# Kernel optimization log

Hardware: AMD Instinct MI355X
Metric: run time of the kernel (lower is better)

Reference implementation:

```python
import jax, jax.numpy as jnp
import numpy as np

B, N, D, H, L = 512, 50000, 64, 600, 200
ALPHA = 1.0
EPS_NORM = 1e-12


def _l2n(x):
    # matches tf.linalg.l2_normalize / keras.backend.l2_normalize (axis=-1)
    return x * jax.lax.rsqrt(jnp.maximum(jnp.sum(x * x, axis=-1, keepdims=True), EPS_NORM))


def setup_inputs() -> dict:
    key = jax.random.key(0)
    ks = jax.random.split(key, 8)
    inputs = jax.random.randint(ks[0], (B, N), 0, 2).astype(jnp.float32)
    item_emb = jax.random.normal(ks[1], (N, D), jnp.float32) * 0.1
    W1 = jax.random.normal(ks[2], (N + D, H), jnp.float32) * 0.01
    Wm = jax.random.normal(ks[3], (H, L), jnp.float32) * 0.05
    Wv = jax.random.normal(ks[4], (H, L), jnp.float32) * 0.05
    Wd1 = jax.random.normal(ks[5], (L, H), jnp.float32) * 0.05
    Wd2 = jax.random.normal(ks[6], (H, N), jnp.float32) * 0.01
    eps = jax.random.normal(ks[7], (B, L), jnp.float32)
    return {
        "inputs": inputs, "item_emb": item_emb,
        "W1": W1, "b1": jnp.zeros((H,), jnp.float32),
        "Wm": Wm, "bm": jnp.zeros((L,), jnp.float32),
        "Wv": Wv, "bv": jnp.zeros((L,), jnp.float32),
        "Wd1": Wd1, "bd1": jnp.zeros((H,), jnp.float32),
        "Wd2": Wd2, "bd2": jnp.zeros((N,), jnp.float32),
        "eps": eps,
    }


def reference(inputs, item_emb, W1, b1, Wm, bm, Wv, bv, Wd1, bd1, Wd2, bd2, eps):
    # --- vectorized replacement of tf.map_fn row-wise masked gather + mean pool ---
    mask = (inputs > 0).astype(inputs.dtype)            # [B, N]
    cnt = jnp.maximum(jnp.sum(mask, axis=-1, keepdims=True), 1.0)
    pooled = (mask @ item_emb) / cnt                    # [B, D] mean of selected item embeddings
    x = jnp.concatenate([inputs, ALPHA * _l2n(pooled)], axis=-1)  # [B, N+D]
    # --- encoder ---
    xn = _l2n(x)                                        # l2 normalize over axis=1
    h = jnp.tanh(xn @ W1 + b1)                          # [B, H]
    z_mean = h @ Wm + bm                                # [B, L]
    z_log_var = h @ Wv + bv                             # [B, L]
    z = z_mean + jnp.exp(0.5 * z_log_var) * eps         # reparameterization
    # --- decoder ---
    reconstructed = jnp.tanh(z @ Wd1 + bd1) @ Wd2 + bd2  # [B, N]
    kl_loss = -0.5 * jnp.mean(z_log_var - jnp.square(z_mean) - jnp.exp(z_log_var) + 1.0)
    return reconstructed, kl_loss
```

## Files before the change

### kernel.cpp

```cpp
#include <hip/hip_runtime.h>

#define BB 512
#define NN 50000
#define DD 64
#define HH 600
#define LL 200

#define K1 50176
#define S1 1568
#define N1P 704
#define NCH 28
#define CKE 1792
#define CW 56
#define NST 14

#define K2P 640
#define N2P 50048

typedef __attribute__((ext_vector_type(8))) short bf16x8;
typedef __attribute__((ext_vector_type(4))) float f32x4;

__device__ __forceinline__ unsigned short f2bf(float f) {
  union { float f; unsigned u; } v; v.f = f;
  unsigned r = v.u + 0x7fffu + ((v.u >> 16) & 1u);
  return (unsigned short)(r >> 16);
}

__device__ __forceinline__ void g2l16(const void* g, void* l) {
  __builtin_amdgcn_global_load_lds((const __attribute__((address_space(1))) unsigned int*)g,
                                   (__attribute__((address_space(3))) unsigned int*)l, 16, 0, 0);
}

__global__ __launch_bounds__(256) void k_prep(const float* __restrict__ inp,
                                              unsigned* __restrict__ maskT,
                                              float* __restrict__ cnt,
                                              float* __restrict__ P,
                                              float* __restrict__ outkl) {
  int b = blockIdx.x, tid = threadIdx.x;
  const float4* row4 = (const float4*)(inp + (size_t)b * NN);
  int c = 0;
  for (int w = tid; w < S1; w += 256) {
    unsigned m = 0;
    int kb = w * 32;
    if (kb + 32 <= NN) {
#pragma unroll
      for (int q = 0; q < 8; ++q) {
        float4 f = row4[w * 8 + q];
        m |= (f.x > 0.5f ? 1u : 0u) << (4 * q);
        m |= (f.y > 0.5f ? 1u : 0u) << (4 * q + 1);
        m |= (f.z > 0.5f ? 1u : 0u) << (4 * q + 2);
        m |= (f.w > 0.5f ? 1u : 0u) << (4 * q + 3);
      }
    } else {
      for (int k = kb; k < NN && k < kb + 32; ++k)
        m |= (inp[(size_t)b * NN + k] > 0.5f ? 1u : 0u) << (k - kb);
    }
    maskT[(size_t)w * BB + b] = m;
    c += __popc(m);
  }
  __shared__ int sred[256];
  sred[tid] = c; __syncthreads();
  for (int s = 128; s > 0; s >>= 1) { if (tid < s) sred[tid] += sred[tid + s]; __syncthreads(); }
  if (tid == 0) cnt[b] = (float)sred[0];
  for (int j = tid; j < N1P; j += 256) P[(size_t)b * N1P + j] = 0.f;
  if (b == 0 && tid == 0) *outkl = 0.f;
}

__global__ __launch_bounds__(256) void k_convB1(const float* __restrict__ W1,
                                                const float* __restrict__ item_emb,
                                                unsigned short* __restrict__ BT) {
  __shared__ unsigned short lds[64][65];
  int k0 = blockIdx.x * 64, j0 = blockIdx.y * 64;
  int tx = threadIdx.x & 63, ty = threadIdx.x >> 6;
  int j = j0 + tx;
#pragma unroll
  for (int r = 0; r < 16; ++r) {
    int k = k0 + ty + 4 * r;
    float v = 0.f;
    if (k < NN) {
      if (j < HH) v = W1[(size_t)k * HH + j];
      else if (j < HH + DD) v = item_emb[(size_t)k * DD + (j - HH)];
    }
    lds[tx][ty + 4 * r] = f2bf(v);
  }
  __syncthreads();
#pragma unroll
  for (int r = 0; r < 16; ++r) {
    int jj = j0 + ty + 4 * r;
    int kk = k0 + tx;
    BT[(size_t)jj * K1 + kk] = lds[ty + 4 * r][tx];
  }
}

__global__ __launch_bounds__(256) void k_convB2(const float* __restrict__ Wd2,
                                                unsigned short* __restrict__ WT) {
  __shared__ unsigned short lds[64][65];
  int n0 = blockIdx.x * 64, k0 = blockIdx.y * 64;
  int tx = threadIdx.x & 63, ty = threadIdx.x >> 6;
  int n = n0 + tx;
#pragma unroll
  for (int r = 0; r < 16; ++r) {
    int k = k0 + ty + 4 * r;
    float v = 0.f;
    if (k < HH && n < NN) v = Wd2[(size_t)k * NN + n];
    lds[tx][ty + 4 * r] = f2bf(v);
  }
  __syncthreads();
#pragma unroll
  for (int r = 0; r < 16; ++r) {
    int nn = n0 + ty + 4 * r;
    int kk = k0 + tx;
    WT[(size_t)nn * K2P + kk] = lds[ty + 4 * r][tx];
  }
}

__global__ __launch_bounds__(512) void k_gemm1(const unsigned* __restrict__ maskT,
                                               const unsigned short* __restrict__ BT,
                                               float* __restrict__ P) {
  __shared__ unsigned short sB[2 * 8192];
  __shared__ unsigned sM[2 * 2048];
  int tid = threadIdx.x;
  int wave = tid >> 6, lane = tid & 63;
  int lr = lane & 15, kg = lane >> 4;
  int n0 = blockIdx.x * 64;
  int m0 = wave * 64;
  int cK = blockIdx.y * CKE;
  int cWo = blockIdx.y * CW;

  auto stage = [&](int p, int st) {
    int kb = cK + st * 128;
#pragma unroll
    for (int i = 0; i < 2; ++i) {
      int row = wave * 8 + i * 4 + kg;
      int cbs = (lr * 16) ^ ((row & 7) << 4);
      const unsigned short* src = BT + (size_t)(n0 + row) * K1 + kb + (cbs >> 1);
      unsigned short* dst = sB + p * 8192 + wave * 1024 + i * 512;
      g2l16(src, dst);
    }
    int w0 = cWo + st * 4;
    const unsigned* msrc = maskT + (size_t)w0 * BB + wave * 256 + lane * 4;
    unsigned* mdst = sM + p * 2048 + wave * 256;
    g2l16(msrc, mdst);
  };

  stage(0, 0);
  f32x4 acc[4][4] = {};

  for (int st = 0; st < NST; ++st) {
    int cur = st & 1;
    if (st + 1 < NST) {
      stage(cur ^ 1, st + 1);
      asm volatile("s_waitcnt vmcnt(3)" ::: "memory");
    } else {
      asm volatile("s_waitcnt vmcnt(0)" ::: "memory");
    }
    __builtin_amdgcn_s_barrier();

    const unsigned short* Bb = sB + cur * 8192;
    const unsigned* Mb = sM + cur * 2048;
#pragma unroll
    for (int ks = 0; ks < 4; ++ks) {
      bf16x8 b[4];
#pragma unroll
      for (int j = 0; j < 4; ++j) {
        int row = j * 16 + lr;
        int cb = (ks * 64 + kg * 16) ^ ((row & 7) << 4);
        b[j] = *(const bf16x8*)(Bb + row * 128 + (cb >> 1));
      }
#pragma unroll
      for (int i = 0; i < 4; ++i) {
        unsigned mw = Mb[ks * 512 + m0 + i * 16 + lr];
        unsigned byt = (mw >> (kg * 8)) & 0xFFu;
        union { unsigned u[4]; bf16x8 v; } au;
#pragma unroll
        for (int p2 = 0; p2 < 4; ++p2) {
          unsigned t = (byt >> (2 * p2)) & 3u;
          t = (t | (t << 15)) & 0x10001u;
          au.u[p2] = t * 0x3F80u;
        }
#pragma unroll
        for (int j = 0; j < 4; ++j)
          acc[i][j] = __builtin_amdgcn_mfma_f32_16x16x32_bf16(au.v, b[j], acc[i][j], 0, 0, 0);
      }
    }
    __builtin_amdgcn_s_barrier();
  }

  int row0 = (lane >> 4) * 4, col = lane & 15;
#pragma unroll
  for (int i = 0; i < 4; ++i)
#pragma unroll
    for (int j = 0; j < 4; ++j)
#pragma unroll
      for (int r = 0; r < 4; ++r)
        atomicAdd(&P[(size_t)(m0 + i * 16 + row0 + r) * N1P + (n0 + j * 16 + col)], acc[i][j][r]);
}

__global__ __launch_bounds__(256) void k_mid(const float* __restrict__ P,
                                             const float* __restrict__ cntb,
                                             const float* __restrict__ W1,
                                             const float* __restrict__ b1,
                                             const float* __restrict__ Wm,
                                             const float* __restrict__ bm,
                                             const float* __restrict__ Wv,
                                             const float* __restrict__ bv,
                                             const float* __restrict__ Wd1,
                                             const float* __restrict__ bd1,
                                             const float* __restrict__ eps,
                                             unsigned short* __restrict__ TB,
                                             float* __restrict__ outkl) {
  int b = blockIdx.x, tid = threadIdx.x;
  __shared__ float pn[DD];
  __shared__ float h[HH];
  __shared__ float z[LL];
  __shared__ float red[1];
  __shared__ float sred[256];

  float cnt = cntb[b];
  if (tid < 64) {
    float pooled = P[(size_t)b * N1P + HH + tid] / fmaxf(cnt, 1.f);
    float s2 = pooled * pooled;
    for (int o = 32; o > 0; o >>= 1) s2 += __shfl_xor(s2, o);
    float pnv = pooled * rsqrtf(fmaxf(s2, 1e-12f));
    pn[tid] = pnv;
    float p2 = pnv * pnv;
    for (int o = 32; o > 0; o >>= 1) p2 += __shfl_xor(p2, o);
    if (tid == 0) red[0] = rsqrtf(fmaxf(cnt + p2, 1e-12f));
  }
  __syncthreads();
  float inv = red[0];

  for (int j = tid; j < HH; j += 256) {
    float corr = 0.f;
#pragma unroll 8
    for (int d = 0; d < DD; ++d) corr += pn[d] * W1[(size_t)(NN + d) * HH + j];
    h[j] = tanhf((P[(size_t)b * N1P + j] + corr) * inv + b1[j]);
  }
  __syncthreads();

  float klp = 0.f;
  for (int l = tid; l < LL; l += 256) {
    float zm = bm[l], zv = bv[l];
    for (int j = 0; j < HH; ++j) {
      float hv = h[j];
      zm += hv * Wm[(size_t)j * LL + l];
      zv += hv * Wv[(size_t)j * LL + l];
    }
    z[l] = zm + expf(0.5f * zv) * eps[(size_t)b * LL + l];
    klp += zv - zm * zm - expf(zv) + 1.f;
  }
  sred[tid] = klp; __syncthreads();
  for (int s = 128; s > 0; s >>= 1) { if (tid < s) sred[tid] += sred[tid + s]; __syncthreads(); }
  if (tid == 0) atomicAdd(outkl, sred[0] * (-0.5f / (float)(BB * LL)));

  for (int j = tid; j < K2P; j += 256) {
    unsigned short o = 0;
    if (j < HH) {
      float acc = bd1[j];
      for (int l = 0; l < LL; ++l) acc += z[l] * Wd1[(size_t)l * HH + j];
      o = f2bf(tanhf(acc));
    }
    TB[(size_t)b * K2P + j] = o;
  }
}

__global__ __launch_bounds__(512) void k_gemm2(const unsigned short* __restrict__ T,
                                               const unsigned short* __restrict__ WT,
                                               const float* __restrict__ bd2,
                                               float* __restrict__ out) {
  __shared__ unsigned short sB[2 * 8192];
  int tid = threadIdx.x;
  int wave = tid >> 6, lane = tid & 63;
  int lr = lane & 15, kg = lane >> 4;
  int n0 = blockIdx.x * 64;
  int m0 = wave * 64;

  auto stage = [&](int p, int st) {
    int kb = st * 128;
#pragma unroll
    for (int i = 0; i < 2; ++i) {
      int row = wave * 8 + i * 4 + kg;
      int cbs = (lr * 16) ^ ((row & 7) << 4);
      const unsigned short* src = WT + (size_t)(n0 + row) * K2P + kb + (cbs >> 1);
      unsigned short* dst = sB + p * 8192 + wave * 1024 + i * 512;
      g2l16(src, dst);
    }
  };

  stage(0, 0);
  f32x4 acc[4][4] = {};

  for (int st = 0; st < 5; ++st) {
    int cur = st & 1;
    if (st + 1 < 5) {
      stage(cur ^ 1, st + 1);
      asm volatile("s_waitcnt vmcnt(2)" ::: "memory");
    } else {
      asm volatile("s_waitcnt vmcnt(0)" ::: "memory");
    }
    __builtin_amdgcn_s_barrier();

    const unsigned short* Bb = sB + cur * 8192;
#pragma unroll
    for (int ks = 0; ks < 4; ++ks) {
      bf16x8 a[4], b[4];
#pragma unroll
      for (int i = 0; i < 4; ++i)
        a[i] = *(const bf16x8*)(T + (size_t)(m0 + i * 16 + lr) * K2P + st * 128 + ks * 32 + kg * 8);
#pragma unroll
      for (int j = 0; j < 4; ++j) {
        int row = j * 16 + lr;
        int cb = (ks * 64 + kg * 16) ^ ((row & 7) << 4);
        b[j] = *(const bf16x8*)(Bb + row * 128 + (cb >> 1));
      }
#pragma unroll
      for (int i = 0; i < 4; ++i)
#pragma unroll
        for (int j = 0; j < 4; ++j)
          acc[i][j] = __builtin_amdgcn_mfma_f32_16x16x32_bf16(a[i], b[j], acc[i][j], 0, 0, 0);
    }
    __builtin_amdgcn_s_barrier();
  }

  int row0 = (lane >> 4) * 4, col = lane & 15;
#pragma unroll
  for (int i = 0; i < 4; ++i)
#pragma unroll
    for (int j = 0; j < 4; ++j) {
      int n = n0 + j * 16 + col;
      if (n < NN) {
        float bias = bd2[n];
#pragma unroll
        for (int r = 0; r < 4; ++r) {
          int m = m0 + i * 16 + row0 + r;
          out[(size_t)m * NN + n] = acc[i][j][r] + bias;
        }
      }
    }
}

extern "C" void kernel_launch(void* const* d_in, const int* in_sizes, int n_in,
                              void* d_out, int out_size, void* d_ws, size_t ws_size,
                              hipStream_t stream) {
  (void)in_sizes; (void)n_in; (void)out_size; (void)ws_size;
  const float* inputs   = (const float*)d_in[0];
  const float* item_emb = (const float*)d_in[1];
  const float* W1  = (const float*)d_in[2];
  const float* b1  = (const float*)d_in[3];
  const float* Wm  = (const float*)d_in[4];
  const float* bm  = (const float*)d_in[5];
  const float* Wv  = (const float*)d_in[6];
  const float* bv  = (const float*)d_in[7];
  const float* Wd1 = (const float*)d_in[8];
  const float* bd1 = (const float*)d_in[9];
  const float* Wd2 = (const float*)d_in[10];
  const float* bd2 = (const float*)d_in[11];
  const float* eps = (const float*)d_in[12];
  float* out = (float*)d_out;

  char* ws = (char*)d_ws;
  unsigned* maskT     = (unsigned*)(ws + 0ull);
  unsigned short* BT1 = (unsigned short*)(ws + 3211264ull);
  unsigned short* W2T = (unsigned short*)(ws + 73859072ull);
  float* P            = (float*)(ws + 137920512ull);
  unsigned short* TB  = (unsigned short*)(ws + 139362304ull);
  float* cnt          = (float*)(ws + 140017664ull);

  float* outkl = out + (size_t)BB * NN;

  k_prep  <<<dim3(BB),       dim3(256), 0, stream>>>(inputs, maskT, cnt, P, outkl);
  k_convB1<<<dim3(784, 11),  dim3(256), 0, stream>>>(W1, item_emb, BT1);
  k_convB2<<<dim3(782, 10),  dim3(256), 0, stream>>>(Wd2, W2T);
  k_gemm1 <<<dim3(11, NCH),  dim3(512), 0, stream>>>(maskT, BT1, P);
  k_mid   <<<dim3(BB),       dim3(256), 0, stream>>>(P, cnt, W1, b1, Wm, bm, Wv, bv, Wd1, bd1, eps, TB, outkl);
  k_gemm2 <<<dim3(782),      dim3(512), 0, stream>>>(TB, W2T, bd2, out);
}
```

Measured before the change: 704.4 us.

## Prefetch mask and A operands into registers, double the K-split chunks

```diff
diff --git a/kernel.cpp b/kernel.cpp
--- a/kernel.cpp
+++ b/kernel.cpp
@@ -9,10 +9,10 @@
 #define K1 50176
 #define S1 1568
 #define N1P 704
-#define NCH 28
-#define CKE 1792
-#define CW 56
-#define NST 14
+#define NCH 56
+#define CKE 896
+#define CW 28
+#define NST 7
 
 #define K2P 640
 #define N2P 50048
@@ -118,7 +118,6 @@
                                                const unsigned short* __restrict__ BT,
                                                float* __restrict__ P) {
   __shared__ unsigned short sB[2 * 8192];
-  __shared__ unsigned sM[2 * 2048];
   int tid = threadIdx.x;
   int wave = tid >> 6, lane = tid & 63;
   int lr = lane & 15, kg = lane >> 4;
@@ -127,37 +126,43 @@
   int cK = blockIdx.y * CKE;
   int cWo = blockIdx.y * CW;
 
-  auto stage = [&](int p, int st) {
+  auto stageB = [&](int p, int st) {
     int kb = cK + st * 128;
 #pragma unroll
     for (int i = 0; i < 2; ++i) {
       int row = wave * 8 + i * 4 + kg;
       int cbs = (lr * 16) ^ ((row & 7) << 4);
-      const unsigned short* src = BT + (size_t)(n0 + row) * K1 + kb + (cbs >> 1);
-      unsigned short* dst = sB + p * 8192 + wave * 1024 + i * 512;
-      g2l16(src, dst);
-    }
+      g2l16(BT + (size_t)(n0 + row) * K1 + kb + (cbs >> 1),
+            sB + p * 8192 + wave * 1024 + i * 512);
+    }
+  };
+  auto loadM = [&](unsigned* mr, int st) {
     int w0 = cWo + st * 4;
-    const unsigned* msrc = maskT + (size_t)w0 * BB + wave * 256 + lane * 4;
-    unsigned* mdst = sM + p * 2048 + wave * 256;
-    g2l16(msrc, mdst);
+#pragma unroll
+    for (int ks = 0; ks < 4; ++ks)
+#pragma unroll
+      for (int i = 0; i < 4; ++i)
+        mr[ks * 4 + i] = maskT[(size_t)(w0 + ks) * BB + m0 + i * 16 + lr];
   };
 
-  stage(0, 0);
+  unsigned mC[16], mN[16];
+  stageB(0, 0);
+  loadM(mC, 0);
   f32x4 acc[4][4] = {};
 
+#pragma unroll
   for (int st = 0; st < NST; ++st) {
     int cur = st & 1;
     if (st + 1 < NST) {
-      stage(cur ^ 1, st + 1);
-      asm volatile("s_waitcnt vmcnt(3)" ::: "memory");
+      stageB(cur ^ 1, st + 1);
+      loadM(mN, st + 1);
+      asm volatile("s_waitcnt vmcnt(18)" ::: "memory");
     } else {
       asm volatile("s_waitcnt vmcnt(0)" ::: "memory");
     }
     __builtin_amdgcn_s_barrier();
 
     const unsigned short* Bb = sB + cur * 8192;
-    const unsigned* Mb = sM + cur * 2048;
 #pragma unroll
     for (int ks = 0; ks < 4; ++ks) {
       bf16x8 b[4];
@@ -169,8 +174,7 @@
       }
 #pragma unroll
       for (int i = 0; i < 4; ++i) {
-        unsigned mw = Mb[ks * 512 + m0 + i * 16 + lr];
-        unsigned byt = (mw >> (kg * 8)) & 0xFFu;
+        unsigned byt = (mC[ks * 4 + i] >> (kg * 8)) & 0xFFu;
         union { unsigned u[4]; bf16x8 v; } au;
 #pragma unroll
         for (int p2 = 0; p2 < 4; ++p2) {
@@ -184,6 +188,8 @@
       }
     }
     __builtin_amdgcn_s_barrier();
+#pragma unroll
+    for (int q = 0; q < 16; ++q) mC[q] = mN[q];
   }
 
   int row0 = (lane >> 4) * 4, col = lane & 15;
@@ -275,26 +281,36 @@
   int n0 = blockIdx.x * 64;
   int m0 = wave * 64;
 
-  auto stage = [&](int p, int st) {
+  auto stageB = [&](int p, int st) {
     int kb = st * 128;
 #pragma unroll
     for (int i = 0; i < 2; ++i) {
       int row = wave * 8 + i * 4 + kg;
       int cbs = (lr * 16) ^ ((row & 7) << 4);
-      const unsigned short* src = WT + (size_t)(n0 + row) * K2P + kb + (cbs >> 1);
-      unsigned short* dst = sB + p * 8192 + wave * 1024 + i * 512;
-      g2l16(src, dst);
+      g2l16(WT + (size_t)(n0 + row) * K2P + kb + (cbs >> 1),
+            sB + p * 8192 + wave * 1024 + i * 512);
     }
   };
-
-  stage(0, 0);
+  auto loadA = [&](bf16x8* a, int st) {
+#pragma unroll
+    for (int ks = 0; ks < 4; ++ks)
+#pragma unroll
+      for (int i = 0; i < 4; ++i)
+        a[ks * 4 + i] = *(const bf16x8*)(T + (size_t)(m0 + i * 16 + lr) * K2P + st * 128 + ks * 32 + kg * 8);
+  };
+
+  bf16x8 aC[16], aN[16];
+  stageB(0, 0);
+  loadA(aC, 0);
   f32x4 acc[4][4] = {};
 
+#pragma unroll
   for (int st = 0; st < 5; ++st) {
     int cur = st & 1;
     if (st + 1 < 5) {
-      stage(cur ^ 1, st + 1);
-      asm volatile("s_waitcnt vmcnt(2)" ::: "memory");
+      stageB(cur ^ 1, st + 1);
+      loadA(aN, st + 1);
+      asm volatile("s_waitcnt vmcnt(18)" ::: "memory");
     } else {
       asm volatile("s_waitcnt vmcnt(0)" ::: "memory");
     }
@@ -303,10 +319,7 @@
     const unsigned short* Bb = sB + cur * 8192;
 #pragma unroll
     for (int ks = 0; ks < 4; ++ks) {
-      bf16x8 a[4], b[4];
-#pragma unroll
-      for (int i = 0; i < 4; ++i)
-        a[i] = *(const bf16x8*)(T + (size_t)(m0 + i * 16 + lr) * K2P + st * 128 + ks * 32 + kg * 8);
+      bf16x8 b[4];
 #pragma unroll
       for (int j = 0; j < 4; ++j) {
         int row = j * 16 + lr;
@@ -317,9 +330,11 @@
       for (int i = 0; i < 4; ++i)
 #pragma unroll
         for (int j = 0; j < 4; ++j)
-          acc[i][j] = __builtin_amdgcn_mfma_f32_16x16x32_bf16(a[i], b[j], acc[i][j], 0, 0, 0);
+          acc[i][j] = __builtin_amdgcn_mfma_f32_16x16x32_bf16(aC[ks * 4 + i], b[j], acc[i][j], 0, 0, 0);
     }
     __builtin_amdgcn_s_barrier();
+#pragma unroll
+    for (int q = 0; q < 16; ++q) aC[q] = aN[q];
   }
 
   int row0 = (lane >> 4) * 4, col = lane & 15;
```

Result: no change. 705.5 us (+0.2%).
